# Kernel tuning notes

Measured on AMD Instinct MI355X. Metric: run time of the kernel, lower is better.

The kernel has to match this reference:

```python
import jax, jax.numpy as jnp
import numpy as np

DEPTH = 2
HEADS = 8
DIM = 512
DIM_HEAD = DIM // HEADS   # 64
LANDMARKS = DIM // 2      # 256
PINV_ITERS = 6
KERNEL = 33               # attn_values_residual_conv_kernel
IN_DIM = 1024
NUM_CLASSES = 2
FF_MULT = 4


def layer_norm(x, g, b, eps=1e-5):
    mu = x.mean(-1, keepdims=True)
    var = ((x - mu) ** 2).mean(-1, keepdims=True)
    return (x - mu) / jnp.sqrt(var + eps) * g + b


def moore_penrose_pinv(x, iters=PINV_ITERS):
    # Newton-Schulz iterative pseudo-inverse (lucidrains nystrom_attention)
    abs_x = jnp.abs(x)
    col = abs_x.sum(-1)
    row = abs_x.sum(-2)
    z = jnp.swapaxes(x, -1, -2) / (jnp.max(col) * jnp.max(row))
    I = jnp.eye(x.shape[-1], dtype=x.dtype)
    for _ in range(iters):
        xz = x @ z
        z = 0.25 * z @ (13 * I - xz @ (15 * I - xz @ (7 * I - xz)))
    return z


def nystrom_attention(x, qkv_w, out_w, out_b, conv_w):
    b, n, _ = x.shape
    m = LANDMARKS
    pad = (m - n % m) % m
    if pad:
        x = jnp.pad(x, ((0, 0), (pad, 0), (0, 0)))
    N = n + pad
    qkv = x @ qkv_w                                 # [b,N,3*h*d]
    q, k, v = jnp.split(qkv, 3, axis=-1)
    sh = lambda t: t.reshape(b, N, HEADS, DIM_HEAD).transpose(0, 2, 1, 3)
    q, k, v = sh(q), sh(k), sh(v)                   # [b,h,N,d]
    q = q * (DIM_HEAD ** -0.5)
    l = N // m
    q_l = q.reshape(b, HEADS, m, l, DIM_HEAD).mean(3)   # [b,h,m,d]
    k_l = k.reshape(b, HEADS, m, l, DIM_HEAD).mean(3)
    attn1 = jax.nn.softmax(jnp.einsum('bhnd,bhmd->bhnm', q, k_l), -1)   # [b,h,N,m]
    attn2 = jax.nn.softmax(jnp.einsum('bhmd,bhld->bhml', q_l, k_l), -1) # [b,h,m,m]
    attn3 = jax.nn.softmax(jnp.einsum('bhmd,bhnd->bhmn', q_l, k), -1)   # [b,h,m,N]
    out = (attn1 @ moore_penrose_pinv(attn2)) @ (attn3 @ v)             # [b,h,N,d]
    # depthwise residual conv over the sequence dim (groups=heads)
    res = jax.lax.conv_general_dilated(
        v, conv_w, window_strides=(1, 1),
        padding=((KERNEL // 2, KERNEL // 2), (0, 0)),
        dimension_numbers=('NCHW', 'OIHW', 'NCHW'),
        feature_group_count=HEADS)
    out = out + res
    out = out.transpose(0, 2, 1, 3).reshape(b, N, HEADS * DIM_HEAD)
    out = out @ out_w + out_b
    return out[:, -n:]


def setup_inputs() -> dict:
    key = jax.random.key(0)
    ks = jax.random.split(key, 16)
    s = 0.02
    D, H = DEPTH, HEADS
    inp = {
        'x': jax.random.normal(ks[0], (2, 16384, IN_DIM), jnp.float32),
        'fc1_w': jax.random.normal(ks[1], (IN_DIM, DIM), jnp.float32) * s,
        'fc1_b': jnp.zeros((DIM,), jnp.float32),
        'ln1_g': jnp.ones((D, DIM), jnp.float32),
        'ln1_b': jnp.zeros((D, DIM), jnp.float32),
        'qkv_w': jax.random.normal(ks[2], (D, DIM, 3 * DIM), jnp.float32) * s,
        'out_w': jax.random.normal(ks[3], (D, DIM, DIM), jnp.float32) * s,
        'out_b': jnp.zeros((D, DIM), jnp.float32),
        'conv_w': jax.random.normal(ks[4], (D, H, 1, KERNEL, 1), jnp.float32) * s,
        'ln2_g': jnp.ones((D, DIM), jnp.float32),
        'ln2_b': jnp.zeros((D, DIM), jnp.float32),
        'ff1_w': jax.random.normal(ks[5], (D, DIM, FF_MULT * DIM), jnp.float32) * s,
        'ff1_b': jnp.zeros((D, FF_MULT * DIM), jnp.float32),
        'ff2_w': jax.random.normal(ks[6], (D, FF_MULT * DIM, DIM), jnp.float32) * s,
        'ff2_b': jnp.zeros((D, DIM), jnp.float32),
        'att1_w': jax.random.normal(ks[7], (DIM, DIM // 4), jnp.float32) * s,
        'att1_b': jnp.zeros((DIM // 4,), jnp.float32),
        'att2_w': jax.random.normal(ks[8], (DIM // 4, 1), jnp.float32) * s,
        'att2_b': jnp.zeros((1,), jnp.float32),
        'fc2_w': jax.random.normal(ks[9], (DIM, NUM_CLASSES), jnp.float32) * s,
        'fc2_b': jnp.zeros((NUM_CLASSES,), jnp.float32),
    }
    return inp


def reference(x, fc1_w, fc1_b, ln1_g, ln1_b, qkv_w, out_w, out_b, conv_w,
              ln2_g, ln2_b, ff1_w, ff1_b, ff2_w, ff2_b,
              att1_w, att1_b, att2_w, att2_b, fc2_w, fc2_b):
    h = jax.nn.relu(x @ fc1_w + fc1_b)                       # [b,n,512]
    for i in range(DEPTH):
        h = h + nystrom_attention(layer_norm(h, ln1_g[i], ln1_b[i]),
                                  qkv_w[i], out_w[i], out_b[i], conv_w[i])
        hn = layer_norm(h, ln2_g[i], ln2_b[i])
        h = h + (jax.nn.gelu(hn @ ff1_w[i] + ff1_b[i], approximate=False)
                 @ ff2_w[i] + ff2_b[i])
    # gated-attention MIL pooling
    a = jnp.tanh(h @ att1_w + att1_b) @ att2_w + att2_b      # [b,n,1]
    a = jax.nn.softmax(jnp.swapaxes(a, 1, 2), -1)            # [b,1,n]
    z = (a @ h)[:, 0]                                        # [b,512]
    logits = z @ fc2_w + fc2_b
    Y_prob = jax.nn.softmax(logits, -1)
    return logits, Y_prob, a
```

## Files before the change

kernel.cpp:

```cpp
#include <hip/hip_runtime.h>
#include <hip/hip_bf16.h>

typedef long long i64;
typedef __hip_bfloat16 bf16;
using short8 = __attribute__((ext_vector_type(8))) short;
using f32x4  = __attribute__((ext_vector_type(4))) float;

#define SEQ    16384
#define DM     512
#define NHEAD  8
#define DH     64
#define LMK    256
#define LSUB   64
#define Q3     1536
#define FFD    2048
#define BATCH  2
#define ROWS   (BATCH * SEQ)

__device__ __forceinline__ float cvt(float v) { return v; }
__device__ __forceinline__ float cvt(bf16 v) { return __bfloat162float(v); }
__device__ __forceinline__ void stc(float* p, float v) { *p = v; }
__device__ __forceinline__ void stc(bf16* p, float v) { *p = __float2bfloat16(v); }

__device__ __forceinline__ float4 ld4(const float* p) { return *(const float4*)p; }
__device__ __forceinline__ float4 ld4(const bf16* p) {
    union { short s[4]; } u; *(int2*)u.s = *(const int2*)p;
    float4 v;
    v.x = cvt(((const bf16*)u.s)[0]); v.y = cvt(((const bf16*)u.s)[1]);
    v.z = cvt(((const bf16*)u.s)[2]); v.w = cvt(((const bf16*)u.s)[3]);
    return v;
}
__device__ __forceinline__ void ld8f(const bf16* p, float* d) {
    union { short8 v; bf16 e[8]; } u;
    u.v = *(const short8*)p;
#pragma unroll
    for (int j = 0; j < 8; j++) d[j] = cvt(u.e[j]);
}

__device__ __forceinline__ float gelu_fast(float v) {
    float u = v * (1.5957691216057308f + 0.07135370154f * v * v);
    float e = __expf(fminf(u, 80.f));
    return v * e * __builtin_amdgcn_rcpf(e + 1.f);
}
__device__ __forceinline__ float tanh_fast(float v) {
    float e = __expf(fminf(2.f * v, 80.f));
    return 1.f - 2.f * __builtin_amdgcn_rcpf(e + 1.f);
}

#define LDS_U32(p) ((__attribute__((address_space(3))) uint32_t*)(p))
#define GLB_U32(p) ((const __attribute__((address_space(1))) uint32_t*)(p))

template<int FM, int FN, int ACT, bool RESID, bool DSUB, int TMODE, typename TC>
__global__ __launch_bounds__(256)
void mfma_gemm_kernel(const bf16* __restrict__ Abase, const bf16* __restrict__ Btbase,
                      TC* __restrict__ Cbase, bf16* __restrict__ Ctbase,
                      const float* __restrict__ bias,
                      int M, int N, int K, int lda, int ldb, int ldc,
                      i64 sAb, i64 sAh, i64 sBb, i64 sBh, i64 sCb, i64 sCh,
                      int nh, float alpha, float beta, float betaT)
{
    constexpr int BM = FM * 32;
    constexpr int BN = FN * 32;
    constexpr int ASL = BM / 8;
    constexpr int NSL = (BM + BN) / 8;
    constexpr int NIT = NSL / 4;
    __shared__ bf16 Al[BM][64];
    __shared__ bf16 Bl[BN][64];

    int nwg  = gridDim.x * gridDim.y * gridDim.z;
    int orig = (blockIdx.z * gridDim.y + blockIdx.y) * gridDim.x + blockIdx.x;
    int qq = nwg >> 3, rr = nwg & 7;
    int xcd = orig & 7, loc = orig >> 3;
    int wid = (xcd < rr ? xcd * (qq + 1) : rr * (qq + 1) + (xcd - rr) * qq) + loc;
    int bx = wid % gridDim.x;
    int t1 = wid / gridDim.x;
    int by = t1 % gridDim.y;
    int bz = t1 / gridDim.y;

    int bb = bz / nh, hh = bz % nh;
    const bf16* A  = Abase  + bb * sAb + hh * sAh;
    const bf16* Bt = Btbase + bb * sBb + hh * sBh;
    TC*         C  = Cbase  + bb * sCb + hh * sCh;
    bf16* Ct = nullptr;
    if (TMODE) Ct = Ctbase + bb * sCb + hh * sCh;

    int tid = threadIdx.x;
    int wave = tid >> 6, lane = tid & 63;
    int wm = (wave >> 1) * (FM * 16), wn = (wave & 1) * (FN * 16);
    int m0 = by * BM, n0 = bx * BN;
    int lr = lane & 15, lq = lane >> 4;
    int srow = lane >> 3;
    int scol = ((lane & 7) ^ srow) * 8;

    const bf16* gsrc[NIT];
    uint32_t* ldst[NIT];
#pragma unroll
    for (int s = 0; s < NIT; s++) {
        int op = wave + s * 4;
        if (op < ASL) {
            gsrc[s] = A + (i64)(m0 + op * 8 + srow) * lda + scol;
            ldst[s] = (uint32_t*)&Al[op * 8][0];
        } else {
            int o2 = op - ASL;
            gsrc[s] = Bt + (i64)(n0 + o2 * 8 + srow) * ldb + scol;
            ldst[s] = (uint32_t*)&Bl[o2 * 8][0];
        }
    }

    f32x4 acc[FM][FN];
#pragma unroll
    for (int i = 0; i < FM; i++)
#pragma unroll
        for (int j = 0; j < FN; j++) acc[i][j] = (f32x4){0.f, 0.f, 0.f, 0.f};

    int c0 = (lq ^ (lr & 7)) * 8;
    int c1 = ((4 | lq) ^ (lr & 7)) * 8;

    for (int k0 = 0; k0 < K; k0 += 64) {
#pragma unroll
        for (int s = 0; s < NIT; s++)
            __builtin_amdgcn_global_load_lds(GLB_U32(gsrc[s] + k0),
                (__attribute__((address_space(3))) uint32_t*)ldst[s], 16, 0, 0);
        __syncthreads();
        {
            short8 af[FM], bfr[FN];
#pragma unroll
            for (int i = 0; i < FM; i++) af[i]  = *(const short8*)&Al[wm + i * 16 + lr][c0];
#pragma unroll
            for (int j = 0; j < FN; j++) bfr[j] = *(const short8*)&Bl[wn + j * 16 + lr][c0];
#pragma unroll
            for (int i = 0; i < FM; i++)
#pragma unroll
                for (int j = 0; j < FN; j++)
                    acc[i][j] = __builtin_amdgcn_mfma_f32_16x16x32_bf16(af[i], bfr[j], acc[i][j], 0, 0, 0);
        }
        {
            short8 af[FM], bfr[FN];
#pragma unroll
            for (int i = 0; i < FM; i++) af[i]  = *(const short8*)&Al[wm + i * 16 + lr][c1];
#pragma unroll
            for (int j = 0; j < FN; j++) bfr[j] = *(const short8*)&Bl[wn + j * 16 + lr][c1];
#pragma unroll
            for (int i = 0; i < FM; i++)
#pragma unroll
                for (int j = 0; j < FN; j++)
                    acc[i][j] = __builtin_amdgcn_mfma_f32_16x16x32_bf16(af[i], bfr[j], acc[i][j], 0, 0, 0);
        }
        __syncthreads();
    }

#pragma unroll
    for (int i = 0; i < FM; i++)
#pragma unroll
        for (int r = 0; r < 4; r++) {
            int m = m0 + wm + i * 16 + lq * 4 + r;
            TC* crow = C + (i64)m * ldc;
#pragma unroll
            for (int j = 0; j < FN; j++) {
                int n = n0 + wn + j * 16 + lr;
                float v = acc[i][j][r] * alpha;
                if (DSUB) v = ((m == n) ? beta : 0.f) - v;
                if (bias) v += bias[n];
                if (ACT == 1) v = fmaxf(v, 0.f);
                else if (ACT == 2) v = gelu_fast(v);
                else if (ACT == 3) v = tanh_fast(v);
                if (RESID) v += cvt(crow[n]);
                stc(&crow[n], v);
                if (TMODE == 1) Ct[(i64)n * ldc + m] = __float2bfloat16(v);
                else if (TMODE == 2) Ct[(i64)n * ldc + m] = __float2bfloat16(((m == n) ? betaT : 0.f) - v);
            }
        }
}

template<int FM, int FN, int ACT, bool RES, typename TC>
static inline void ml(hipStream_t st, const bf16* A, const bf16* Bt, TC* C, const float* bias,
                      int M, int N, int K, int lda, int ldb, int ldc,
                      i64 sAb = 0, i64 sAh = 0, i64 sBb = 0, i64 sBh = 0, i64 sCb = 0, i64 sCh = 0,
                      int nb = 1, int nh = 1, float alpha = 1.f)
{
    dim3 g(N / (FN * 32), M / (FM * 32), nb * nh);
    mfma_gemm_kernel<FM, FN, ACT, RES, false, 0, TC><<<g, 256, 0, st>>>(
        A, Bt, C, nullptr, bias, M, N, K, lda, ldb, ldc, sAb, sAh, sBb, sBh, sCb, sCh, nh, alpha, 0.f, 0.f);
}

template<int TMODE, bool DSUB>
static inline void mlp2(hipStream_t st, bf16* C, bf16* Ct, const bf16* A, const bf16* Bt,
                        float alpha, float beta = 0.f, float betaT = 0.f)
{
    dim3 g(4, 4, 16);
    mfma_gemm_kernel<2, 2, 0, false, DSUB, TMODE, bf16><<<g, 256, 0, st>>>(
        A, Bt, C, Ct, nullptr, 256, 256, 256, 256, 256, 256,
        0, 65536, 0, 65536, 0, 65536, 16, alpha, beta, betaT);
}

__global__ __launch_bounds__(256)
void attn3_fused_kernel(const bf16* __restrict__ qkv, const bf16* __restrict__ q_lb,
                        const bf16* __restrict__ vTall,
                        float* __restrict__ obuf, float* __restrict__ mbuf,
                        float* __restrict__ sbuf2)
{
    __shared__ bf16 qs[256][64];
    __shared__ bf16 ks[64][64];
    __shared__ bf16 vs[64][64];
    __shared__ bf16 Ps[4][64][64];

    int ch = blockIdx.x, bh = blockIdx.y;
    int b = bh >> 3, hh = bh & 7;
    const bf16* qg = q_lb + (i64)bh * (LMK * DH);
    const bf16* kg = qkv + (i64)b * SEQ * Q3 + DM + hh * DH;
    const bf16* vg = vTall + ((i64)b * NHEAD + hh) * ((i64)DH * SEQ);

    int tid = threadIdx.x;
    int wave = tid >> 6, lane = tid & 63;
    int lr = lane & 15, lq = lane >> 4;
    int srow = lane >> 3;
    int scol = ((lane & 7) ^ srow) * 8;
    int c0 = (lq ^ (lr & 7)) * 8;
    int c1 = ((4 | lq) ^ (lr & 7)) * 8;
    int qb = wave * 64;

    for (int sl = wave; sl < 32; sl += 4)
        __builtin_amdgcn_global_load_lds(GLB_U32(qg + (i64)(sl * 8 + srow) * 64 + scol),
                                         LDS_U32(&qs[sl * 8][0]), 16, 0, 0);

    f32x4 O[4][4];
    float m[4][4], s[4][4];
#pragma unroll
    for (int i = 0; i < 4; i++)
#pragma unroll
        for (int r = 0; r < 4; r++) { m[i][r] = -3.0e38f; s[i][r] = 0.f; }
#pragma unroll
    for (int i = 0; i < 4; i++)
#pragma unroll
        for (int j = 0; j < 4; j++) O[i][j] = (f32x4){0.f, 0.f, 0.f, 0.f};

    int k0g = ch * 1024;
    for (int t = 0; t < 16; t++) {
        int kk0 = k0g + t * 64;
        for (int sl = wave; sl < 8; sl += 4)
            __builtin_amdgcn_global_load_lds(GLB_U32(kg + (i64)(kk0 + sl * 8 + srow) * Q3 + scol),
                                             LDS_U32(&ks[sl * 8][0]), 16, 0, 0);
        for (int sl = wave; sl < 8; sl += 4)
            __builtin_amdgcn_global_load_lds(GLB_U32(vg + (i64)(sl * 8 + srow) * SEQ + kk0 + scol),
                                             LDS_U32(&vs[sl * 8][0]), 16, 0, 0);
        __syncthreads();

        f32x4 S[4][4];
#pragma unroll
        for (int i = 0; i < 4; i++)
#pragma unroll
            for (int j = 0; j < 4; j++) S[i][j] = (f32x4){0.f, 0.f, 0.f, 0.f};
        {
            short8 af[4], bk[4];
#pragma unroll
            for (int i = 0; i < 4; i++) af[i] = *(const short8*)&qs[qb + i * 16 + lr][c0];
#pragma unroll
            for (int j = 0; j < 4; j++) bk[j] = *(const short8*)&ks[j * 16 + lr][c0];
#pragma unroll
            for (int i = 0; i < 4; i++)
#pragma unroll
                for (int j = 0; j < 4; j++)
                    S[i][j] = __builtin_amdgcn_mfma_f32_16x16x32_bf16(af[i], bk[j], S[i][j], 0, 0, 0);
#pragma unroll
            for (int i = 0; i < 4; i++) af[i] = *(const short8*)&qs[qb + i * 16 + lr][c1];
#pragma unroll
            for (int j = 0; j < 4; j++) bk[j] = *(const short8*)&ks[j * 16 + lr][c1];
#pragma unroll
            for (int i = 0; i < 4; i++)
#pragma unroll
                for (int j = 0; j < 4; j++)
                    S[i][j] = __builtin_amdgcn_mfma_f32_16x16x32_bf16(af[i], bk[j], S[i][j], 0, 0, 0);
        }

#pragma unroll
        for (int i = 0; i < 4; i++)
#pragma unroll
            for (int r = 0; r < 4; r++) {
                float tm = -3.0e38f;
#pragma unroll
                for (int j = 0; j < 4; j++) {
                    S[i][j][r] *= 0.125f;
                    tm = fmaxf(tm, S[i][j][r]);
                }
                tm = fmaxf(tm, __shfl_xor(tm, 1)); tm = fmaxf(tm, __shfl_xor(tm, 2));
                tm = fmaxf(tm, __shfl_xor(tm, 4)); tm = fmaxf(tm, __shfl_xor(tm, 8));
                float mn = fmaxf(m[i][r], tm);
                float f = expf(m[i][r] - mn);
                float ss = 0.f;
#pragma unroll
                for (int j = 0; j < 4; j++) {
                    float e = expf(S[i][j][r] - mn);
                    S[i][j][r] = e;
                    ss += e;
                }
                ss += __shfl_xor(ss, 1); ss += __shfl_xor(ss, 2);
                ss += __shfl_xor(ss, 4); ss += __shfl_xor(ss, 8);
                s[i][r] = s[i][r] * f + ss;
                m[i][r] = mn;
#pragma unroll
                for (int j2 = 0; j2 < 4; j2++) O[i][j2][r] *= f;
            }

#pragma unroll
        for (int i = 0; i < 4; i++)
#pragma unroll
            for (int j = 0; j < 4; j++)
#pragma unroll
                for (int r = 0; r < 4; r++) {
                    int row = i * 16 + lq * 4 + r;
                    int col = j * 16 + lr;
                    Ps[wave][row][(((col >> 3) ^ (row & 7)) << 3) | (col & 7)] =
                        __float2bfloat16(S[i][j][r]);
                }
        __syncthreads();

        {
            short8 a2[4], b2[4];
#pragma unroll
            for (int i = 0; i < 4; i++) a2[i] = *(const short8*)&Ps[wave][i * 16 + lr][c0];
#pragma unroll
            for (int j = 0; j < 4; j++) b2[j] = *(const short8*)&vs[j * 16 + lr][c0];
#pragma unroll
            for (int i = 0; i < 4; i++)
#pragma unroll
                for (int j = 0; j < 4; j++)
                    O[i][j] = __builtin_amdgcn_mfma_f32_16x16x32_bf16(a2[i], b2[j], O[i][j], 0, 0, 0);
#pragma unroll
            for (int i = 0; i < 4; i++) a2[i] = *(const short8*)&Ps[wave][i * 16 + lr][c1];
#pragma unroll
            for (int j = 0; j < 4; j++) b2[j] = *(const short8*)&vs[j * 16 + lr][c1];
#pragma unroll
            for (int i = 0; i < 4; i++)
#pragma unroll
                for (int j = 0; j < 4; j++)
                    O[i][j] = __builtin_amdgcn_mfma_f32_16x16x32_bf16(a2[i], b2[j], O[i][j], 0, 0, 0);
        }
        __syncthreads();
    }

    i64 base = (i64)(bh * 16 + ch) * 256 * 64;
#pragma unroll
    for (int i = 0; i < 4; i++)
#pragma unroll
        for (int j2 = 0; j2 < 4; j2++)
#pragma unroll
            for (int r = 0; r < 4; r++) {
                int row = qb + i * 16 + lq * 4 + r;
                int d = j2 * 16 + lr;
                obuf[base + (i64)row * 64 + d] = O[i][j2][r];
            }
    if (lr == 0) {
#pragma unroll
        for (int i = 0; i < 4; i++)
#pragma unroll
            for (int r = 0; r < 4; r++) {
                int idx = (bh * 16 + ch) * 256 + qb + i * 16 + lq * 4 + r;
                mbuf[idx] = m[i][r];
                sbuf2[idx] = s[i][r];
            }
    }
}

__global__ __launch_bounds__(256)
void attn3_combine_kernel(const float* __restrict__ obuf, const float* __restrict__ mbuf,
                          const float* __restrict__ sbuf2, bf16* __restrict__ a3vT)
{
    int gid = blockIdx.x * 4 + (threadIdx.x >> 6);
    int lane = threadIdx.x & 63;
    int bh = gid >> 8, row = gid & 255;
    float mv[16];
    float M = -3.0e38f;
#pragma unroll
    for (int c = 0; c < 16; c++) {
        mv[c] = mbuf[(bh * 16 + c) * 256 + row];
        M = fmaxf(M, mv[c]);
    }
    float denom = 0.f, w[16];
#pragma unroll
    for (int c = 0; c < 16; c++) {
        w[c] = expf(mv[c] - M);
        denom += sbuf2[(bh * 16 + c) * 256 + row] * w[c];
    }
    float acc = 0.f;
#pragma unroll
    for (int c = 0; c < 16; c++)
        acc += obuf[((i64)(bh * 16 + c) * 256 + row) * 64 + lane] * w[c];
    a3vT[(i64)bh * (DH * LMK) + lane * 256 + row] = __float2bfloat16(acc / denom);
}

__global__ __launch_bounds__(256)
void attn1_fused_kernel(const bf16* __restrict__ qkv, const bf16* __restrict__ klb_all,
                        const bf16* __restrict__ yTb_all, bf16* __restrict__ xn)
{
    __shared__ bf16 stage[20480];
    __shared__ bf16 Ps[64][256];
    __shared__ float maxb[2][64];
    __shared__ float sumb[2][64];
    bf16 (*qs)[64]  = (bf16(*)[64])&stage[0];
    bf16 (*ks)[64]  = (bf16(*)[64])&stage[4096];
    bf16 (*yts)[256]= (bf16(*)[256])&stage[0];

    int hh = blockIdx.y;
    i64 g0 = (i64)blockIdx.x * 64;
    int b  = (int)(g0 >> 14);
    const bf16* qg = qkv + (i64)b * SEQ * Q3 + (g0 & (SEQ - 1)) * Q3 + hh * DH;
    const bf16* kg = klb_all + (i64)(b * NHEAD + hh) * (LMK * DH);
    const bf16* yg = yTb_all + (i64)(b * NHEAD + hh) * (DH * LMK);

    int tid = threadIdx.x;
    int wave = tid >> 6, lane = tid & 63;
    int lr = lane & 15, lq = lane >> 4;
    int srow = lane >> 3;
    int scol = ((lane & 7) ^ srow) * 8;

    for (int sl = wave; sl < 8; sl += 4)
        __builtin_amdgcn_global_load_lds(GLB_U32(qg + (i64)(sl * 8 + srow) * Q3 + scol),
                                         LDS_U32(&qs[sl * 8][0]), 16, 0, 0);
    for (int sl = wave; sl < 32; sl += 4)
        __builtin_amdgcn_global_load_lds(GLB_U32(kg + (i64)(sl * 8 + srow) * 64 + scol),
                                         LDS_U32(&ks[sl * 8][0]), 16, 0, 0);
    __syncthreads();

    int wm = (wave >> 1) * 32, wn = (wave & 1) * 128;
    f32x4 acc[2][8];
#pragma unroll
    for (int i = 0; i < 2; i++)
#pragma unroll
        for (int j = 0; j < 8; j++) acc[i][j] = (f32x4){0.f, 0.f, 0.f, 0.f};

    int c0 = (lq ^ (lr & 7)) * 8;
    int c1 = ((4 | lq) ^ (lr & 7)) * 8;
    {
        short8 af[2], bfr[8];
#pragma unroll
        for (int i = 0; i < 2; i++) af[i]  = *(const short8*)&qs[wm + i * 16 + lr][c0];
#pragma unroll
        for (int j = 0; j < 8; j++) bfr[j] = *(const short8*)&ks[wn + j * 16 + lr][c0];
#pragma unroll
        for (int i = 0; i < 2; i++)
#pragma unroll
            for (int j = 0; j < 8; j++)
                acc[i][j] = __builtin_amdgcn_mfma_f32_16x16x32_bf16(af[i], bfr[j], acc[i][j], 0, 0, 0);
    }
    {
        short8 af[2], bfr[8];
#pragma unroll
        for (int i = 0; i < 2; i++) af[i]  = *(const short8*)&qs[wm + i * 16 + lr][c1];
#pragma unroll
        for (int j = 0; j < 8; j++) bfr[j] = *(const short8*)&ks[wn + j * 16 + lr][c1];
#pragma unroll
        for (int i = 0; i < 2; i++)
#pragma unroll
            for (int j = 0; j < 8; j++)
                acc[i][j] = __builtin_amdgcn_mfma_f32_16x16x32_bf16(af[i], bfr[j], acc[i][j], 0, 0, 0);
    }

#pragma unroll
    for (int i = 0; i < 2; i++)
#pragma unroll
        for (int j = 0; j < 8; j++)
#pragma unroll
            for (int r = 0; r < 4; r++) acc[i][j][r] *= 0.125f;
#pragma unroll
    for (int i = 0; i < 2; i++)
#pragma unroll
        for (int r = 0; r < 4; r++) {
            float m = acc[i][0][r];
#pragma unroll
            for (int j = 1; j < 8; j++) m = fmaxf(m, acc[i][j][r]);
            m = fmaxf(m, __shfl_xor(m, 1)); m = fmaxf(m, __shfl_xor(m, 2));
            m = fmaxf(m, __shfl_xor(m, 4)); m = fmaxf(m, __shfl_xor(m, 8));
            if (lr == 0) maxb[wave & 1][wm + i * 16 + lq * 4 + r] = m;
        }
    __syncthreads();

    {
        int r2 = lane >> 5, c32 = lane & 31;
        for (int sl = wave; sl < 32; sl += 4) {
            int row = sl * 2 + r2;
            const bf16* g = yg + (i64)row * 256 + ((c32 ^ (row & 7)) * 8);
            __builtin_amdgcn_global_load_lds(GLB_U32(g), LDS_U32(&yts[sl * 2][0]), 16, 0, 0);
        }
    }

#pragma unroll
    for (int i = 0; i < 2; i++)
#pragma unroll
        for (int r = 0; r < 4; r++) {
            int row = wm + i * 16 + lq * 4 + r;
            float fm = fmaxf(maxb[0][row], maxb[1][row]);
            float ss = 0.f;
#pragma unroll
            for (int j = 0; j < 8; j++) {
                float e = expf(acc[i][j][r] - fm);
                acc[i][j][r] = e;
                ss += e;
            }
            ss += __shfl_xor(ss, 1); ss += __shfl_xor(ss, 2);
            ss += __shfl_xor(ss, 4); ss += __shfl_xor(ss, 8);
            if (lr == 0) sumb[wave & 1][row] = ss;
        }
#pragma unroll
    for (int i = 0; i < 2; i++)
#pragma unroll
        for (int j = 0; j < 8; j++)
#pragma unroll
            for (int r = 0; r < 4; r++) {
                int row = wm + i * 16 + lq * 4 + r;
                int col = wn + j * 16 + lr;
                Ps[row][(((col >> 3) ^ (row & 7)) << 3) | (col & 7)] = __float2bfloat16(acc[i][j][r]);
            }
    __syncthreads();

    float s[2][4];
#pragma unroll
    for (int i = 0; i < 2; i++)
#pragma unroll
        for (int r = 0; r < 4; r++) {
            int row = wm + i * 16 + lq * 4 + r;
            s[i][r] = sumb[0][row] + sumb[1][row];
        }

    int wn2 = (wave & 1) * 32;
    f32x4 acc2[2][2];
#pragma unroll
    for (int i = 0; i < 2; i++)
#pragma unroll
        for (int j = 0; j < 2; j++) acc2[i][j] = (f32x4){0.f, 0.f, 0.f, 0.f};
#pragma unroll
    for (int kk = 0; kk < 8; kk++) {
        int cc = ((kk * 4 + lq) ^ (lr & 7)) * 8;
        short8 a2[2], b2[2];
#pragma unroll
        for (int i = 0; i < 2; i++) a2[i] = *(const short8*)&Ps[wm + i * 16 + lr][cc];
#pragma unroll
        for (int j = 0; j < 2; j++) b2[j] = *(const short8*)&yts[wn2 + j * 16 + lr][cc];
#pragma unroll
        for (int i = 0; i < 2; i++)
#pragma unroll
            for (int j = 0; j < 2; j++)
                acc2[i][j] = __builtin_amdgcn_mfma_f32_16x16x32_bf16(a2[i], b2[j], acc2[i][j], 0, 0, 0);
    }

#pragma unroll
    for (int i = 0; i < 2; i++)
#pragma unroll
        for (int j = 0; j < 2; j++)
#pragma unroll
            for (int r = 0; r < 4; r++) {
                int row = wm + i * 16 + lq * 4 + r;
                int d = wn2 + j * 16 + lr;
                xn[(g0 + row) * DM + hh * DH + d] = __float2bfloat16(acc2[i][j][r] / s[i][r]);
            }
}

__global__ __launch_bounds__(256)
void transpose_w_kernel(const float* __restrict__ in, bf16* __restrict__ out, int K, int N)
{
    __shared__ float t[64][65];
    int k0 = blockIdx.y * 64, n0 = blockIdx.x * 64;
    int c = threadIdx.x & 63, r4 = threadIdx.x >> 6;
#pragma unroll
    for (int p = 0; p < 64; p += 4)
        t[p + r4][c] = in[(i64)(k0 + p + r4) * N + n0 + c];
    __syncthreads();
#pragma unroll
    for (int p = 0; p < 64; p += 4)
        out[(i64)(n0 + p + r4) * K + k0 + c] = __float2bfloat16(t[c][p + r4]);
}

__global__ __launch_bounds__(256)
void t64_kernel(const bf16* __restrict__ in, bf16* __restrict__ out, int ldin, int ldout,
                i64 sIb, i64 sIh, i64 sOb, i64 sOh, int nh)
{
    __shared__ bf16 t[64][72];
    int zz = blockIdx.y;
    int bb = zz / nh, hh = zz % nh;
    const bf16* ip = in + bb * sIb + hh * sIh;
    bf16* op = out + bb * sOb + hh * sOh;
    int r0 = blockIdx.x * 64;
    int c = threadIdx.x & 63, r4 = threadIdx.x >> 6;
#pragma unroll
    for (int p = 0; p < 64; p += 4)
        t[p + r4][c] = ip[(i64)(r0 + p + r4) * ldin + c];
    __syncthreads();
#pragma unroll
    for (int p = 0; p < 64; p += 4)
        op[(i64)(p + r4) * ldout + r0 + c] = t[c][p + r4];
}

__global__ void cvt_bf16_kernel(const float* __restrict__ in, bf16* __restrict__ out, i64 n)
{
    i64 i = ((i64)blockIdx.x * 256 + threadIdx.x) * 4;
    if (i >= n) return;
    float4 v = *(const float4*)&in[i];
    out[i + 0] = __float2bfloat16(v.x);
    out[i + 1] = __float2bfloat16(v.y);
    out[i + 2] = __float2bfloat16(v.z);
    out[i + 3] = __float2bfloat16(v.w);
}

__global__ __launch_bounds__(256)
void ln_kernel(const bf16* __restrict__ in, bf16* __restrict__ out,
               const float* __restrict__ g, const float* __restrict__ b, int nrows)
{
    int row = blockIdx.x * 4 + (threadIdx.x >> 6);
    int lane = threadIdx.x & 63;
    if (row >= nrows) return;
    const bf16* x = in + (i64)row * DM;
    float vv[8];
    ld8f(&x[lane * 8], vv);
    float s = 0.f;
#pragma unroll
    for (int j = 0; j < 8; j++) s += vv[j];
    for (int o = 32; o > 0; o >>= 1) s += __shfl_xor(s, o);
    float mu = s * (1.f / DM);
    float dd[8];
#pragma unroll
    for (int j = 0; j < 8; j++) dd[j] = vv[j] - mu;
    float vs = 0.f;
#pragma unroll
    for (int j = 0; j < 8; j++) vs += dd[j] * dd[j];
    for (int o = 32; o > 0; o >>= 1) vs += __shfl_xor(vs, o);
    float rstd = rsqrtf(vs * (1.f / DM) + 1e-5f);
    int c = lane * 8;
    bf16* y = out + (i64)row * DM;
#pragma unroll
    for (int j = 0; j < 8; j++)
        y[c + j] = __float2bfloat16(dd[j] * rstd * g[c + j] + b[c + j]);
}

__global__ void landmark_kernel(const bf16* __restrict__ qkv, bf16* __restrict__ q_lb,
                                bf16* __restrict__ klb)
{
    int blk = blockIdx.x;
    int which = blk >> 12;
    int blk2 = blk & 4095;
    int im = blk2 & (LMK - 1);
    int bh = blk2 >> 8;
    int b = bh >> 3, h = bh & 7;
    int d = threadIdx.x;
    int off = which ? DM : 0;
    const bf16* p = qkv + (i64)(b * SEQ + im * LSUB) * Q3 + off + h * DH + d;
    float s = 0.f;
    for (int il = 0; il < LSUB; il++) s += cvt(p[(i64)il * Q3]);
    bf16* out = which ? klb : q_lb;
    out[((i64)bh * LMK + im) * DH + d] = __float2bfloat16(s * (1.f / LSUB));
}

__global__ __launch_bounds__(256)
void softmax256_fb_kernel(const float* __restrict__ in, bf16* __restrict__ out, i64 nrows)
{
    i64 row = (i64)blockIdx.x * 4 + (threadIdx.x >> 6);
    int lane = threadIdx.x & 63;
    if (row >= nrows) return;
    const float* p = in + row * 256;
    float4 v = *(const float4*)&p[lane * 4];
    float mx = fmaxf(fmaxf(v.x, v.y), fmaxf(v.z, v.w));
    for (int o = 32; o > 0; o >>= 1) mx = fmaxf(mx, __shfl_xor(mx, o));
    v.x = expf(v.x - mx); v.y = expf(v.y - mx);
    v.z = expf(v.z - mx); v.w = expf(v.w - mx);
    float s = v.x + v.y + v.z + v.w;
    for (int o = 32; o > 0; o >>= 1) s += __shfl_xor(s, o);
    float inv = 1.f / s;
    bf16* q = out + row * 256;
    q[lane * 4 + 0] = __float2bfloat16(v.x * inv);
    q[lane * 4 + 1] = __float2bfloat16(v.y * inv);
    q[lane * 4 + 2] = __float2bfloat16(v.z * inv);
    q[lane * 4 + 3] = __float2bfloat16(v.w * inv);
}

__global__ __launch_bounds__(256)
void softmax_big_kernel(const float* __restrict__ in, float* __restrict__ out)
{
    __shared__ float buf[SEQ];
    __shared__ float red[256];
    int t = threadIdx.x;
    const float* src = in + (i64)blockIdx.x * SEQ;
    float mx = -3.0e38f;
#pragma unroll
    for (int j = 0; j < 16; j++) {
        float4 v = *(const float4*)&src[(j * 256 + t) * 4];
        *(float4*)&buf[(j * 256 + t) * 4] = v;
        mx = fmaxf(mx, fmaxf(fmaxf(v.x, v.y), fmaxf(v.z, v.w)));
    }
    red[t] = mx; __syncthreads();
    for (int s = 128; s > 0; s >>= 1) { if (t < s) red[t] = fmaxf(red[t], red[t + s]); __syncthreads(); }
    mx = red[0];
    __syncthreads();
    float sum = 0.f;
#pragma unroll
    for (int j = 0; j < 16; j++) {
        float4 v = *(float4*)&buf[(j * 256 + t) * 4];
        v.x = expf(v.x - mx); v.y = expf(v.y - mx);
        v.z = expf(v.z - mx); v.w = expf(v.w - mx);
        *(float4*)&buf[(j * 256 + t) * 4] = v;
        sum += v.x + v.y + v.z + v.w;
    }
    red[t] = sum; __syncthreads();
    for (int s = 128; s > 0; s >>= 1) { if (t < s) red[t] += red[t + s]; __syncthreads(); }
    float inv = 1.f / red[0];
    float* dst = out + (i64)blockIdx.x * SEQ;
#pragma unroll
    for (int j = 0; j < 16; j++) {
        float4 v = *(float4*)&buf[(j * 256 + t) * 4];
        v.x *= inv; v.y *= inv; v.z *= inv; v.w *= inv;
        *(float4*)&dst[(j * 256 + t) * 4] = v;
    }
}

__global__ void pinv_sums_kernel(const bf16* __restrict__ x, float* __restrict__ scal)
{
    int bh = blockIdx.x;
    const bf16* p = x + (i64)bh * 65536;
    int t = threadIdx.x;
    float cs = 0.f, rs = 0.f;
    for (int i = 0; i < 256; i++) cs += fabsf(cvt(p[i * 256 + t]));
    for (int j = 0; j < 256; j++) rs += fabsf(cvt(p[t * 256 + j]));
    __shared__ float rc[256], rr[256];
    rc[t] = cs; rr[t] = rs; __syncthreads();
    for (int s = 128; s > 0; s >>= 1) {
        if (t < s) { rc[t] = fmaxf(rc[t], rc[t + s]); rr[t] = fmaxf(rr[t], rr[t + s]); }
        __syncthreads();
    }
    if (t == 0) {
        atomicMax(reinterpret_cast<int*>(&scal[0]), __float_as_int(rc[0]));
        atomicMax(reinterpret_cast<int*>(&scal[1]), __float_as_int(rr[0]));
    }
}

__global__ void pinv_init_kernel(const bf16* __restrict__ x, const float* __restrict__ scal,
                                 bf16* __restrict__ z, bf16* __restrict__ zT)
{
    i64 idx = (i64)blockIdx.x * 256 + threadIdx.x;
    int j = (int)(idx & 255); int i = (int)((idx >> 8) & 255); i64 bh = idx >> 16;
    float inv = 1.f / (scal[0] * scal[1]);
    float xv = cvt(x[idx]) * inv;
    zT[idx] = __float2bfloat16(xv);
    z[(bh << 16) + ((i64)j << 8) + i] = __float2bfloat16(xv);
}

__global__ __launch_bounds__(256)
void conv_add_kernel(const bf16* __restrict__ qkv, const float* __restrict__ w,
                     bf16* __restrict__ xn)
{
    union U8 { short8 v; bf16 e[8]; };
    i64 idx = (i64)blockIdx.x * 256 + threadIdx.x;
    int cg = (int)(idx & 63);
    i64 bn = idx >> 6;
    int n = (int)(bn & (SEQ - 1));
    int b = (int)(bn >> 14);
    int c = cg * 8;
    int h = c >> 6;

    U8 xin; xin.v = *(const short8*)&xn[(bn << 9) + c];
    float acc[8];
#pragma unroll
    for (int j = 0; j < 8; j++) acc[j] = cvt(xin.e[j]);

    const float* wk = w + h * 33;
    const bf16* vb = qkv + (i64)b * SEQ * Q3 + 2 * DM + c;
#pragma unroll
    for (int t = 0; t < 33; t++) {
        int nn = n + t - 16;
        if (nn >= 0 && nn < SEQ) {
            U8 vv; vv.v = *(const short8*)&vb[(i64)nn * Q3];
            float wt = wk[t];
#pragma unroll
            for (int j = 0; j < 8; j++) acc[j] = fmaf(wt, cvt(vv.e[j]), acc[j]);
        }
    }
    U8 o;
#pragma unroll
    for (int j = 0; j < 8; j++) o.e[j] = __float2bfloat16(acc[j]);
    *(short8*)&xn[(bn << 9) + c] = o.v;
}

__global__ void pool_score_kernel(const float* __restrict__ t, const float* __restrict__ w,
                                  const float* __restrict__ b2, float* __restrict__ s)
{
    int row = blockIdx.x * 4 + (threadIdx.x >> 6);
    int lane = threadIdx.x & 63;
    float acc = t[(i64)row * 128 + lane] * w[lane] + t[(i64)row * 128 + 64 + lane] * w[64 + lane];
    for (int o = 32; o > 0; o >>= 1) acc += __shfl_xor(acc, o);
    if (lane == 0) s[row] = acc + b2[0];
}

__global__ __launch_bounds__(256)
void pool_z_kernel(const float* __restrict__ a, const bf16* __restrict__ h, float* __restrict__ z)
{
    int bb = blockIdx.x >> 7, cg = blockIdx.x & 127;
    int c4 = cg * 4;
    int t = threadIdx.x;
    const float* ab = a + (i64)bb * SEQ;
    const bf16* hb = h + (i64)bb * SEQ * DM;
    float4 acc = {0.f, 0.f, 0.f, 0.f};
    for (int r = t; r < SEQ; r += 256) {
        float av = ab[r];
        float4 hv = ld4(&hb[(i64)r * DM + c4]);
        acc.x += av * hv.x; acc.y += av * hv.y; acc.z += av * hv.z; acc.w += av * hv.w;
    }
    __shared__ float4 red[256];
    red[t] = acc; __syncthreads();
    for (int s = 128; s > 0; s >>= 1) {
        if (t < s) {
            float4 o = red[t + s];
            red[t].x += o.x; red[t].y += o.y; red[t].z += o.z; red[t].w += o.w;
        }
        __syncthreads();
    }
    if (t == 0) *(float4*)&z[bb * DM + c4] = red[0];
}

__global__ void head_kernel(const float* __restrict__ z, const float* __restrict__ w,
                            const float* __restrict__ b, float* __restrict__ out)
{
    int t = threadIdx.x;
    int wv = t >> 6, lane = t & 63;
    int bb = wv >> 1, cls = wv & 1;
    float acc = 0.f;
#pragma unroll
    for (int j = 0; j < 8; j++) { int k = lane * 8 + j; acc += z[bb * DM + k] * w[k * 2 + cls]; }
    for (int o = 32; o > 0; o >>= 1) acc += __shfl_xor(acc, o);
    __shared__ float lg[4];
    if (lane == 0) lg[wv] = acc + b[cls];
    __syncthreads();
    if (t == 0) {
        for (int bi = 0; bi < 2; bi++) {
            float l0 = lg[bi * 2], l1 = lg[bi * 2 + 1];
            out[bi * 2 + 0] = l0; out[bi * 2 + 1] = l1;
            float m = fmaxf(l0, l1);
            float e0 = expf(l0 - m), e1 = expf(l1 - m);
            float inv = 1.f / (e0 + e1);
            out[4 + bi * 2 + 0] = e0 * inv; out[4 + bi * 2 + 1] = e1 * inv;
        }
    }
}

extern "C" void kernel_launch(void* const* d_in, const int* in_sizes, int n_in,
                              void* d_out, int out_size, void* d_ws, size_t ws_size,
                              hipStream_t stream)
{
    const float* x      = (const float*)d_in[0];
    const float* fc1_w  = (const float*)d_in[1];
    const float* fc1_b  = (const float*)d_in[2];
    const float* ln1_g  = (const float*)d_in[3];
    const float* ln1_b  = (const float*)d_in[4];
    const float* qkv_w  = (const float*)d_in[5];
    const float* out_w  = (const float*)d_in[6];
    const float* out_b  = (const float*)d_in[7];
    const float* conv_w = (const float*)d_in[8];
    const float* ln2_g  = (const float*)d_in[9];
    const float* ln2_b  = (const float*)d_in[10];
    const float* ff1_w  = (const float*)d_in[11];
    const float* ff1_b  = (const float*)d_in[12];
    const float* ff2_w  = (const float*)d_in[13];
    const float* ff2_b  = (const float*)d_in[14];
    const float* att1_w = (const float*)d_in[15];
    const float* att1_b = (const float*)d_in[16];
    const float* att2_w = (const float*)d_in[17];
    const float* att2_b = (const float*)d_in[18];
    const float* fc2_w  = (const float*)d_in[19];
    const float* fc2_b  = (const float*)d_in[20];
    float* out = (float*)d_out;
    float* ws  = (float*)d_ws;

    i64 off = 0;
    bf16*  h    = (bf16*)(ws + off); off += (i64)ROWS * DM;
    bf16*  xn   = (bf16*)(ws + off); off += (i64)ROWS * DM / 2;
    bf16*  qkv  = (bf16*)(ws + off); off += (i64)ROWS * Q3 / 2;
    float* sbuf = ws + off; off += (i64)2 * LMK * SEQ;
    float* attn2= ws + off; off += 16 * 65536;
    float* zA   = ws + off; off += 16 * 65536;
    float* zB   = ws + off; off += 16 * 65536;
    float* xz   = ws + off; off += 16 * 65536;
    float* wbuf = ws + off; off += 16 * 65536;
    float* tbuf = ws + off; off += 16 * 65536;
    float* regK = ws + off; off += 16 * LMK * DH;
    float* regL = ws + off; off += 16 * LMK * DH;
    float* a3v  = ws + off; off += 16 * LMK * DH;
    float* ybuf = ws + off; off += 16 * LMK * DH;
    float* scor = ws + off; off += ROWS;
    float* zpool= ws + off; off += BATCH * DM;
    float* scal = ws + off; off += 16;
    if (ws_size < (size_t)off * sizeof(float)) return;

    bf16*  wT   = (bf16*)sbuf;
    bf16*  xb   = qkv;
    float* attn2f = attn2;
    bf16*  attn2b = (bf16*)zA;
    bf16*  XZ     = (bf16*)(zA + 524288);
    bf16*  zG     = (bf16*)zB;
    bf16*  zGT    = (bf16*)(zB + 524288);
    bf16*  zH     = (bf16*)xz;
    bf16*  zHT    = (bf16*)(xz + 524288);
    bf16*  W1     = (bf16*)wbuf;
    bf16*  W2     = (bf16*)(wbuf + 524288);
    bf16*  zF     = attn2b;
    bf16*  vTall = (bf16*)sbuf;
    float* obuf  = zB;
    float* mbuf  = ybuf;
    float* sbuf2 = ybuf + 65536;
    bf16*  a3vTb = (bf16*)a3v;
    bf16*  q_lb = (bf16*)regK;
    bf16*  klb  = (bf16*)(regK + 131072);
    bf16*  yTb  = (bf16*)regL;
    bf16*  wTa  = (bf16*)(regL + 131072);
    bf16*  wTf1 = (bf16*)attn2;
    bf16*  wTf2 = (bf16*)zA;
    bf16*  ffc  = qkv;

    const i64 sQKVb = (i64)SEQ * Q3;
    const i64 sLMh  = (i64)LMK * DH;

    cvt_bf16_kernel<<<(ROWS * 1024 / 4 + 255) / 256, 256, 0, stream>>>(x, xb, (i64)ROWS * 1024);
    transpose_w_kernel<<<dim3(DM / 64, 1024 / 64), 256, 0, stream>>>(fc1_w, wT, 1024, DM);
    ml<4, 2, 1, false>(stream, xb, wT, h, fc1_b, ROWS, DM, 1024, 1024, 1024, DM);

    for (int L = 0; L < 2; L++) {
        const float* qw  = qkv_w + (i64)L * DM * Q3;
        const float* ow  = out_w + (i64)L * DM * DM;
        const float* ob  = out_b + (i64)L * DM;
        const float* cw  = conv_w + (i64)L * NHEAD * 33;
        const float* f1w = ff1_w + (i64)L * DM * FFD;
        const float* f1b = ff1_b + (i64)L * FFD;
        const float* f2w = ff2_w + (i64)L * FFD * DM;
        const float* f2b = ff2_b + (i64)L * DM;

        ln_kernel<<<ROWS/4, 256, 0, stream>>>(h, xn, ln1_g + L*DM, ln1_b + L*DM, ROWS);
        transpose_w_kernel<<<dim3(Q3 / 64, DM / 64), 256, 0, stream>>>(qw, wT, DM, Q3);
        ml<4, 2, 0, false>(stream, xn, wT, qkv, nullptr, ROWS, Q3, DM, DM, DM, Q3);

        landmark_kernel<<<2*16*LMK, 64, 0, stream>>>(qkv, q_lb, klb);

        ml<2, 2, 0, false>(stream, q_lb, klb, attn2f, nullptr,
            LMK, LMK, DH, DH, DH, LMK, 0, sLMh, 0, sLMh, 0, 65536, 1, 16, 0.125f);
        softmax256_fb_kernel<<<16*LMK/4, 256, 0, stream>>>(attn2f, attn2b, (i64)16*LMK);

        hipMemsetAsync(scal, 0, 2*sizeof(float), stream);
        pinv_sums_kernel<<<16, 256, 0, stream>>>(attn2b, scal);
        pinv_init_kernel<<<16*65536/256, 256, 0, stream>>>(attn2b, scal, zG, zGT);
        {
            bf16 *zp = zG, *zpT = zGT, *zq = zH, *zqT = zHT;
            for (int it = 0; it < 6; it++) {
                bool last = (it == 5);
                mlp2<2, false>(stream, XZ, W1, attn2b, zpT, 1.f, 0.f, 7.f);
                mlp2<0, true >(stream, W2, nullptr, W1, XZ, 1.f, 15.f);
                mlp2<0, true >(stream, W1, nullptr, W2, XZ, 1.f, 13.f);
                if (!last) {
                    mlp2<1, false>(stream, zq, zqT, zp, W1, 0.25f);
                    bf16* t1 = zp; zp = zq; zq = t1;
                    bf16* t2 = zpT; zpT = zqT; zqT = t2;
                } else {
                    mlp2<0, false>(stream, zF, nullptr, zp, W1, 0.25f);
                }
            }
        }

        t64_kernel<<<dim3(SEQ/64, BATCH*NHEAD), 256, 0, stream>>>(
            qkv + 2*DM, vTall, Q3, SEQ,
            sQKVb, (i64)DH, (i64)NHEAD*DH*SEQ, (i64)DH*SEQ, NHEAD);
        attn3_fused_kernel<<<dim3(16, 16), 256, 0, stream>>>(qkv, q_lb, vTall, obuf, mbuf, sbuf2);
        attn3_combine_kernel<<<16*LMK/4, 256, 0, stream>>>(obuf, mbuf, sbuf2, a3vTb);

        ml<2, 4, 0, false>(stream, a3vTb, zF, yTb, nullptr,
            DH, LMK, LMK, LMK, LMK, LMK, 0, (i64)DH*LMK, 0, 65536, 0, (i64)DH*LMK, 1, 16, 1.f);

        attn1_fused_kernel<<<dim3(ROWS/64, NHEAD), 256, 0, stream>>>(qkv, klb, yTb, xn);

        conv_add_kernel<<<(i64)ROWS*64/256, 256, 0, stream>>>(qkv, cw, xn);
        transpose_w_kernel<<<dim3(DM / 64, DM / 64), 256, 0, stream>>>(ow, wT, DM, DM);
        ml<4, 2, 0, true>(stream, xn, wT, h, ob, ROWS, DM, DM, DM, DM, DM);

        ln_kernel<<<ROWS/4, 256, 0, stream>>>(h, xn, ln2_g + L*DM, ln2_b + L*DM, ROWS);
        transpose_w_kernel<<<dim3(FFD / 64, DM / 64), 256, 0, stream>>>(f1w, wTf1, DM, FFD);
        transpose_w_kernel<<<dim3(DM / 64, FFD / 64), 256, 0, stream>>>(f2w, wTf2, FFD, DM);
        ml<4, 2, 2, false>(stream, xn, wTf1, ffc, f1b, ROWS, FFD, DM, DM, DM, FFD);
        ml<4, 2, 0, true >(stream, ffc, wTf2, h, f2b, ROWS, DM, FFD, FFD, FFD, DM);
    }

    transpose_w_kernel<<<dim3(128 / 64, DM / 64), 256, 0, stream>>>(att1_w, wTa, DM, 128);
    ml<4, 2, 3, false>(stream, h, wTa, sbuf, att1_b, ROWS, 128, DM, DM, DM, 128);
    pool_score_kernel<<<ROWS/4, 256, 0, stream>>>(sbuf, att2_w, att2_b, scor);
    softmax_big_kernel<<<BATCH, 256, 0, stream>>>(scor, out + 8);
    pool_z_kernel<<<BATCH * 128, 256, 0, stream>>>(out + 8, h, zpool);
    head_kernel<<<1, 256, 0, stream>>>(zpool, fc2_w, fc2_b, out);
}
```

Measured before the change: 1.852 ms.

## Split attn3 into more chunks, store bf16 partials, use fast exp, specialize conv

The attn3 split-K kernel now uses 32 chunks of 512 keys instead of 16 chunks of 1024, doubling the grid from 256 to 512 blocks to occupy more of the GPU. Its partial outputs are stored in bf16 to halve the traffic to and from the combine kernel, and the combine loop is rewritten to match. expf is replaced by __expf in several softmax kernels. The residual conv gets a bounds-check-free path for interior rows, and the landmark-mean loop is unrolled. bf16 partials and the fast exp lose some accuracy.

```diff
diff --git a/kernel.cpp b/kernel.cpp
--- a/kernel.cpp
+++ b/kernel.cpp
@@ -196,7 +196,7 @@
 __global__ __launch_bounds__(256)
 void attn3_fused_kernel(const bf16* __restrict__ qkv, const bf16* __restrict__ q_lb,
                         const bf16* __restrict__ vTall,
-                        float* __restrict__ obuf, float* __restrict__ mbuf,
+                        bf16* __restrict__ obuf, float* __restrict__ mbuf,
                         float* __restrict__ sbuf2)
 {
     __shared__ bf16 qs[256][64];
@@ -234,8 +234,8 @@
 #pragma unroll
         for (int j = 0; j < 4; j++) O[i][j] = (f32x4){0.f, 0.f, 0.f, 0.f};
 
-    int k0g = ch * 1024;
-    for (int t = 0; t < 16; t++) {
+    int k0g = ch * 512;
+    for (int t = 0; t < 8; t++) {
         int kk0 = k0g + t * 64;
         for (int sl = wave; sl < 8; sl += 4)
             __builtin_amdgcn_global_load_lds(GLB_U32(kg + (i64)(kk0 + sl * 8 + srow) * Q3 + scol),
@@ -285,11 +285,11 @@
                 tm = fmaxf(tm, __shfl_xor(tm, 1)); tm = fmaxf(tm, __shfl_xor(tm, 2));
                 tm = fmaxf(tm, __shfl_xor(tm, 4)); tm = fmaxf(tm, __shfl_xor(tm, 8));
                 float mn = fmaxf(m[i][r], tm);
-                float f = expf(m[i][r] - mn);
+                float f = __expf(m[i][r] - mn);
                 float ss = 0.f;
 #pragma unroll
                 for (int j = 0; j < 4; j++) {
-                    float e = expf(S[i][j][r] - mn);
+                    float e = __expf(S[i][j][r] - mn);
                     S[i][j][r] = e;
                     ss += e;
                 }
@@ -338,7 +338,7 @@
         __syncthreads();
     }
 
-    i64 base = (i64)(bh * 16 + ch) * 256 * 64;
+    i64 base = (i64)(bh * 32 + ch) * 256 * 64;
 #pragma unroll
     for (int i = 0; i < 4; i++)
 #pragma unroll
@@ -347,14 +347,14 @@
             for (int r = 0; r < 4; r++) {
                 int row = qb + i * 16 + lq * 4 + r;
                 int d = j2 * 16 + lr;
-                obuf[base + (i64)row * 64 + d] = O[i][j2][r];
+                obuf[base + (i64)row * 64 + d] = __float2bfloat16(O[i][j2][r]);
             }
     if (lr == 0) {
 #pragma unroll
         for (int i = 0; i < 4; i++)
 #pragma unroll
             for (int r = 0; r < 4; r++) {
-                int idx = (bh * 16 + ch) * 256 + qb + i * 16 + lq * 4 + r;
+                int idx = (bh * 32 + ch) * 256 + qb + i * 16 + lq * 4 + r;
                 mbuf[idx] = m[i][r];
                 sbuf2[idx] = s[i][r];
             }
@@ -362,29 +362,24 @@
 }
 
 __global__ __launch_bounds__(256)
-void attn3_combine_kernel(const float* __restrict__ obuf, const float* __restrict__ mbuf,
+void attn3_combine_kernel(const bf16* __restrict__ obuf, const float* __restrict__ mbuf,
                           const float* __restrict__ sbuf2, bf16* __restrict__ a3vT)
 {
     int gid = blockIdx.x * 4 + (threadIdx.x >> 6);
     int lane = threadIdx.x & 63;
     int bh = gid >> 8, row = gid & 255;
-    float mv[16];
+    const float* mrow = mbuf + (i64)(bh * 32) * 256 + row;
+    const float* srow = sbuf2 + (i64)(bh * 32) * 256 + row;
     float M = -3.0e38f;
 #pragma unroll
-    for (int c = 0; c < 16; c++) {
-        mv[c] = mbuf[(bh * 16 + c) * 256 + row];
-        M = fmaxf(M, mv[c]);
-    }
-    float denom = 0.f, w[16];
-#pragma unroll
-    for (int c = 0; c < 16; c++) {
-        w[c] = expf(mv[c] - M);
-        denom += sbuf2[(bh * 16 + c) * 256 + row] * w[c];
-    }
-    float acc = 0.f;
-#pragma unroll
-    for (int c = 0; c < 16; c++)
-        acc += obuf[((i64)(bh * 16 + c) * 256 + row) * 64 + lane] * w[c];
+    for (int c = 0; c < 32; c++) M = fmaxf(M, mrow[c * 256]);
+    float denom = 0.f, acc = 0.f;
+#pragma unroll
+    for (int c = 0; c < 32; c++) {
+        float w = __expf(mrow[c * 256] - M);
+        denom += srow[c * 256] * w;
+        acc += cvt(obuf[((i64)(bh * 32 + c) * 256 + row) * 64 + lane]) * w;
+    }
     a3vT[(i64)bh * (DH * LMK) + lane * 256 + row] = __float2bfloat16(acc / denom);
 }
 
@@ -492,7 +487,7 @@
             float ss = 0.f;
 #pragma unroll
             for (int j = 0; j < 8; j++) {
-                float e = expf(acc[i][j][r] - fm);
+                float e = __expf(acc[i][j][r] - fm);
                 acc[i][j][r] = e;
                 ss += e;
             }
@@ -643,6 +638,7 @@
     int off = which ? DM : 0;
     const bf16* p = qkv + (i64)(b * SEQ + im * LSUB) * Q3 + off + h * DH + d;
     float s = 0.f;
+#pragma unroll 8
     for (int il = 0; il < LSUB; il++) s += cvt(p[(i64)il * Q3]);
     bf16* out = which ? klb : q_lb;
     out[((i64)bh * LMK + im) * DH + d] = __float2bfloat16(s * (1.f / LSUB));
@@ -658,8 +654,8 @@
     float4 v = *(const float4*)&p[lane * 4];
     float mx = fmaxf(fmaxf(v.x, v.y), fmaxf(v.z, v.w));
     for (int o = 32; o > 0; o >>= 1) mx = fmaxf(mx, __shfl_xor(mx, o));
-    v.x = expf(v.x - mx); v.y = expf(v.y - mx);
-    v.z = expf(v.z - mx); v.w = expf(v.w - mx);
+    v.x = __expf(v.x - mx); v.y = __expf(v.y - mx);
+    v.z = __expf(v.z - mx); v.w = __expf(v.w - mx);
     float s = v.x + v.y + v.z + v.w;
     for (int o = 32; o > 0; o >>= 1) s += __shfl_xor(s, o);
     float inv = 1.f / s;
@@ -692,8 +688,8 @@
 #pragma unroll
     for (int j = 0; j < 16; j++) {
         float4 v = *(float4*)&buf[(j * 256 + t) * 4];
-        v.x = expf(v.x - mx); v.y = expf(v.y - mx);
-        v.z = expf(v.z - mx); v.w = expf(v.w - mx);
+        v.x = __expf(v.x - mx); v.y = __expf(v.y - mx);
+        v.z = __expf(v.z - mx); v.w = __expf(v.w - mx);
         *(float4*)&buf[(j * 256 + t) * 4] = v;
         sum += v.x + v.y + v.z + v.w;
     }
@@ -760,14 +756,25 @@
 
     const float* wk = w + h * 33;
     const bf16* vb = qkv + (i64)b * SEQ * Q3 + 2 * DM + c;
-#pragma unroll
-    for (int t = 0; t < 33; t++) {
-        int nn = n + t - 16;
-        if (nn >= 0 && nn < SEQ) {
-            U8 vv; vv.v = *(const short8*)&vb[(i64)nn * Q3];
+    if (n >= 16 && n < SEQ - 16) {
+        const bf16* vb0 = vb + (i64)(n - 16) * Q3;
+#pragma unroll
+        for (int t = 0; t < 33; t++) {
+            U8 vv; vv.v = *(const short8*)&vb0[(i64)t * Q3];
             float wt = wk[t];
 #pragma unroll
             for (int j = 0; j < 8; j++) acc[j] = fmaf(wt, cvt(vv.e[j]), acc[j]);
+        }
+    } else {
+#pragma unroll
+        for (int t = 0; t < 33; t++) {
+            int nn = n + t - 16;
+            if (nn >= 0 && nn < SEQ) {
+                U8 vv; vv.v = *(const short8*)&vb[(i64)nn * Q3];
+                float wt = wk[t];
+#pragma unroll
+                for (int j = 0; j < 8; j++) acc[j] = fmaf(wt, cvt(vv.e[j]), acc[j]);
+            }
         }
     }
     U8 o;
@@ -898,9 +905,9 @@
     bf16*  W2     = (bf16*)(wbuf + 524288);
     bf16*  zF     = attn2b;
     bf16*  vTall = (bf16*)sbuf;
-    float* obuf  = zB;
+    bf16*  obufb = (bf16*)zB;
     float* mbuf  = ybuf;
-    float* sbuf2 = ybuf + 65536;
+    float* sbuf2 = ybuf + 131072;
     bf16*  a3vTb = (bf16*)a3v;
     bf16*  q_lb = (bf16*)regK;
     bf16*  klb  = (bf16*)(regK + 131072);
@@ -960,8 +967,8 @@
         t64_kernel<<<dim3(SEQ/64, BATCH*NHEAD), 256, 0, stream>>>(
             qkv + 2*DM, vTall, Q3, SEQ,
             sQKVb, (i64)DH, (i64)NHEAD*DH*SEQ, (i64)DH*SEQ, NHEAD);
-        attn3_fused_kernel<<<dim3(16, 16), 256, 0, stream>>>(qkv, q_lb, vTall, obuf, mbuf, sbuf2);
-        attn3_combine_kernel<<<16*LMK/4, 256, 0, stream>>>(obuf, mbuf, sbuf2, a3vTb);
+        attn3_fused_kernel<<<dim3(32, 16), 256, 0, stream>>>(qkv, q_lb, vTall, obufb, mbuf, sbuf2);
+        attn3_combine_kernel<<<16*LMK/4, 256, 0, stream>>>(obufb, mbuf, sbuf2, a3vTb);
 
         ml<2, 4, 0, false>(stream, a3vTb, zF, yTb, nullptr,
             DH, LMK, LMK, LMK, LMK, LMK, 0, (i64)DH*LMK, 0, 65536, 0, (i64)DH*LMK, 1, 16, 1.f);
```

Result: faster. 1.757 ms (-5.1%).
